# Kernel optimization log

Measured on AMD Instinct MI355X. Metric: run time of the kernel, lower is better.

## Reference

```python
import jax, jax.numpy as jnp
import numpy as np

B, S, H, NH = 2, 2048, 1024, 16
HD = H // NH


def setup_inputs() -> dict:
    key = jax.random.key(0)
    ks = jax.random.split(key, 12)
    query = jax.random.normal(ks[0], (B, S, H), dtype=jnp.float32)
    key_t = jax.random.normal(ks[1], (B, S, H), dtype=jnp.float32)
    value = jax.random.normal(ks[2], (B, S, H), dtype=jnp.float32)
    kpm = jax.random.randint(ks[3], (B, S), 0, 2).astype(bool)
    kpm = kpm.at[:, 0].set(False)  # guarantee at least one unmasked key per row
    bias = jax.random.normal(ks[4], (1, NH, S, S), dtype=jnp.float32)
    init = 0.02
    q_w = jax.random.normal(ks[5], (H, H), dtype=jnp.float32) * init
    k_w = jax.random.normal(ks[6], (H, H), dtype=jnp.float32) * init
    v_w = jax.random.normal(ks[7], (H, H), dtype=jnp.float32) * init
    o_w = jax.random.normal(ks[8], (H, H), dtype=jnp.float32) * init
    q_b = jnp.zeros((H,), jnp.float32)
    k_b = jnp.zeros((H,), jnp.float32)
    v_b = jnp.zeros((H,), jnp.float32)
    o_b = jnp.zeros((H,), jnp.float32)
    return {"query": query, "key": key_t, "value": value,
            "key_padding_mask": kpm, "bias": bias,
            "q_w": q_w, "q_b": q_b, "k_w": k_w, "k_b": k_b,
            "v_w": v_w, "v_b": v_b, "o_w": o_w, "o_b": o_b}


def _shape(x):
    # [B, S, H] -> [B, NH, S, HD]
    b, s, _ = x.shape
    return x.reshape(b, s, NH, HD).transpose(0, 2, 1, 3)


def reference(query, key, value, key_padding_mask, bias,
              q_w, q_b, k_w, k_b, v_w, v_b, o_w, o_b):
    scale = HD ** -0.5
    q = _shape(query @ q_w.T + q_b)
    k = _shape(key @ k_w.T + k_b)
    v = _shape(value @ v_w.T + v_b)
    attn = jnp.einsum('bhqd,bhkd->bhqk', q, k) * scale + bias
    mask = key_padding_mask[:, None, None, :]  # [B,1,1,S]
    attn = jnp.where(mask, -jnp.inf, attn)
    probs = jax.nn.softmax(attn, axis=-1)
    # safe-softmax: zero masked entries and renormalize with clamped denom
    probs = jnp.where(mask, 0.0, probs)
    denom = jnp.maximum(probs.sum(axis=-1, keepdims=True), 1e-6)
    probs = probs / denom
    ctx = jnp.einsum('bhqk,bhkd->bhqd', probs, v)
    ctx = ctx.transpose(0, 2, 1, 3).reshape(query.shape[0], query.shape[1], H)
    return ctx @ o_w.T + o_b
```

## Files before the change

kernel.cpp:

```cpp
#include <hip/hip_runtime.h>
#include <math.h>

#define Ss  2048
#define Hh  1024

typedef unsigned short u16;
typedef __attribute__((ext_vector_type(8))) short short8;
typedef __attribute__((ext_vector_type(4))) float fx4;

__device__ __forceinline__ u16 f2bf(float f) {
  unsigned int u = __float_as_uint(f);
  u = (u + 0x7fffu + ((u >> 16) & 1u)) >> 16;
  return (u16)u;
}

__device__ __forceinline__ void gld_lds16(const u16* g, u16* l) {
  __builtin_amdgcn_global_load_lds(
      (const __attribute__((address_space(1))) unsigned int*)(const unsigned int*)g,
      (__attribute__((address_space(3))) unsigned int*)(unsigned int*)l, 16, 0, 0);
}

#define MFMA16(a,b,c) __builtin_amdgcn_mfma_f32_16x16x32_bf16((a),(b),(c),0,0,0)

__global__ __launch_bounds__(256) void cast3(const float* __restrict__ a,
    const float* __restrict__ b, const float* __restrict__ c,
    u16* __restrict__ oa, u16* __restrict__ ob, u16* __restrict__ oc) {
  const int z = blockIdx.z;
  const float* in = z == 0 ? a : (z == 1 ? b : c);
  u16* out = z == 0 ? oa : (z == 1 ? ob : oc);
  const int i = (blockIdx.x * 256 + threadIdx.x) * 4;
  const float4 v = *(const float4*)(in + i);
  ushort4 r; r.x = f2bf(v.x); r.y = f2bf(v.y); r.z = f2bf(v.z); r.w = f2bf(v.w);
  *(ushort4*)(out + i) = r;
}

__global__ __launch_bounds__(256) void cast4(const float* __restrict__ a,
    const float* __restrict__ b, const float* __restrict__ c, const float* __restrict__ d,
    u16* __restrict__ oa, u16* __restrict__ ob, u16* __restrict__ oc, u16* __restrict__ od) {
  const int z = blockIdx.z;
  const float* in = z == 0 ? a : (z == 1 ? b : (z == 2 ? c : d));
  u16* out = z == 0 ? oa : (z == 1 ? ob : (z == 2 ? oc : od));
  const int i = (blockIdx.x * 256 + threadIdx.x) * 4;
  const float4 v = *(const float4*)(in + i);
  ushort4 r; r.x = f2bf(v.x); r.y = f2bf(v.y); r.z = f2bf(v.z); r.w = f2bf(v.w);
  *(ushort4*)(out + i) = r;
}

__global__ __launch_bounds__(256) void build_maskadd(const int* __restrict__ kpm,
                                                     float* __restrict__ ma) {
  const int i = blockIdx.x * 256 + threadIdx.x;
  ma[i] = kpm[i] ? -1.0e30f : 0.0f;
}

template <int MODE>
__device__ __forceinline__ void gemm_core(const u16* __restrict__ A,
    const u16* __restrict__ W, const float* __restrict__ bias,
    void* __restrict__ out, float scale) {
  __shared__ __align__(16) u16 As[2][4096];
  __shared__ __align__(16) u16 Bs[2][4096];
  const int tid = threadIdx.x;
  const int w = tid >> 6, lane = tid & 63, ln = lane & 15, quad = lane >> 4;
  const int i0 = blockIdx.y * 128, j0 = blockIdx.x * 128;
  const int wr = (w & 1) * 64, wc = (w >> 1) * 64;
  fx4 acc[4][4] = {};
  const int L0 = w * 64 + lane, L1 = L0 + 256;
  const u16* sa0 = A + (size_t)(i0 + (L0 & 127)) * 1024 + (L0 >> 7) * 8;
  const u16* sa1 = A + (size_t)(i0 + (L1 & 127)) * 1024 + (L1 >> 7) * 8;
  const u16* sb0 = W + (size_t)(j0 + (L0 & 127)) * 1024 + (L0 >> 7) * 8;
  const u16* sb1 = W + (size_t)(j0 + (L1 & 127)) * 1024 + (L1 >> 7) * 8;
  const int d0 = (w * 64) * 8, d1 = (256 + w * 64) * 8;

  gld_lds16(sa0, &As[0][d0]); gld_lds16(sa1, &As[0][d1]);
  gld_lds16(sb0, &Bs[0][d0]); gld_lds16(sb1, &Bs[0][d1]);
  __syncthreads();

  for (int k0 = 0; k0 < 1024; k0 += 32) {
    const int cur = (k0 >> 5) & 1;
    if (k0 + 32 < 1024) {
      const int nb = cur ^ 1;
      gld_lds16(sa0 + k0 + 32, &As[nb][d0]); gld_lds16(sa1 + k0 + 32, &As[nb][d1]);
      gld_lds16(sb0 + k0 + 32, &Bs[nb][d0]); gld_lds16(sb1 + k0 + 32, &Bs[nb][d1]);
    }
    short8 a[4], b[4];
#pragma unroll
    for (int t = 0; t < 4; ++t) {
      a[t] = *(const short8*)&As[cur][(quad * 128 + wr + t * 16 + ln) * 8];
      b[t] = *(const short8*)&Bs[cur][(quad * 128 + wc + t * 16 + ln) * 8];
    }
#pragma unroll
    for (int mt = 0; mt < 4; ++mt)
#pragma unroll
      for (int nt = 0; nt < 4; ++nt)
        acc[mt][nt] = MFMA16(a[mt], b[nt], acc[mt][nt]);
    __syncthreads();
  }
#pragma unroll
  for (int nt = 0; nt < 4; ++nt) {
    const int col = j0 + wc + nt * 16 + ln;
    const float bv = bias[col];
#pragma unroll
    for (int mt = 0; mt < 4; ++mt)
#pragma unroll
      for (int r = 0; r < 4; ++r) {
        const int row = i0 + wr + mt * 16 + quad * 4 + r;
        const float val = (acc[mt][nt][r] + bv) * scale;
        if (MODE == 1) {
          const int bb = row >> 11, s = row & 2047, h = col >> 6, d = col & 63;
          ((u16*)out)[((size_t)(bb * 16 + h) * 2048 + s) * 64 + d] = f2bf(val);
        } else {
          ((float*)out)[(size_t)row * 1024 + col] = val;
        }
      }
  }
}

__global__ __launch_bounds__(256) void gemm_qkv(
    const u16* xq, const u16* xk, const u16* xv,
    const u16* wq, const u16* wk, const u16* wv,
    const float* bq, const float* bk, const float* bv,
    u16* q, u16* k, u16* v) {
  const int z = blockIdx.z;
  const u16* A = z == 0 ? xq : (z == 1 ? xk : xv);
  const u16* W = z == 0 ? wq : (z == 1 ? wk : wv);
  const float* bb = z == 0 ? bq : (z == 1 ? bk : bv);
  u16* o = z == 0 ? q : (z == 1 ? k : v);
  const float sc = z == 0 ? 0.125f : 1.0f;
  gemm_core<1>(A, W, bb, o, sc);
}

__global__ __launch_bounds__(256) void gemm_o(const u16* ctx, const u16* wo,
                                              const float* ob, float* out) {
  gemm_core<0>(ctx, wo, ob, out, 1.0f);
}

__global__ __launch_bounds__(256) void transpose_v(const u16* __restrict__ v,
                                                   u16* __restrict__ vt) {
  __shared__ u16 T[64][72];
  const int tid = threadIdx.x;
  const int bh = blockIdx.y, s0 = blockIdx.x * 64;
#pragma unroll
  for (int i = 0; i < 2; ++i) {
    const int L = i * 256 + tid, key = L >> 3, dc = L & 7;
    const uint4 val = *(const uint4*)&v[((size_t)bh * 2048 + s0 + key) * 64 + dc * 8];
    *(uint4*)&T[key][dc * 8] = val;
  }
  __syncthreads();
#pragma unroll
  for (int i = 0; i < 2; ++i) {
    const int L = i * 256 + tid, d = L >> 3, kc = L & 7;
    u16 tmp[8];
#pragma unroll
    for (int j = 0; j < 8; ++j) tmp[j] = T[kc * 8 + j][d];
    *(uint4*)&vt[((size_t)bh * 64 + d) * 2048 + s0 + kc * 8] = *(const uint4*)tmp;
  }
}

__global__ __launch_bounds__(256) void attn(const u16* __restrict__ Qb,
    const u16* __restrict__ Kb, const u16* __restrict__ VT,
    const float* __restrict__ bias, const float* __restrict__ maskadd,
    u16* __restrict__ ctx) {
  __shared__ __align__(16) u16 Ks[2][4096];
  __shared__ __align__(16) u16 Vs[2][4096];
  __shared__ __align__(16) u16 Ps[4096];
  const int tid = threadIdx.x;
  const int w = tid >> 6, lane = tid & 63, ln = lane & 15, quad = lane >> 4;
  const int q0 = blockIdx.x * 64;
  const int hb = blockIdx.y, h = hb >> 1, b = hb & 1, bh = b * 16 + h;
  const int wr = w * 16;

  short8 qf[2];
#pragma unroll
  for (int ks = 0; ks < 2; ++ks)
    qf[ks] = *(const short8*)&Qb[((size_t)bh * 2048 + q0 + wr + ln) * 64 +
                                 ks * 32 + quad * 8];
  float mi = -3.0e38f, li = 0.f;
  fx4 O[4] = {};

  const int L0 = w * 64 + lane, L1 = L0 + 256;
  const u16* sk0 = Kb + ((size_t)bh * 2048 + (L0 & 63)) * 64 + (L0 >> 6) * 8;
  const u16* sk1 = Kb + ((size_t)bh * 2048 + (L1 & 63)) * 64 + (L1 >> 6) * 8;
  const u16* sv0 = VT + ((size_t)bh * 64 + (L0 & 63)) * 2048 + (L0 >> 6) * 8;
  const u16* sv1 = VT + ((size_t)bh * 64 + (L1 & 63)) * 2048 + (L1 >> 6) * 8;
  const int d0 = (w * 64) * 8, d1 = (256 + w * 64) * 8;

  const float* bp = bias + (size_t)h * Ss * Ss + (size_t)(q0 + wr + ln) * Ss + quad * 4;
  const float* mp = maskadd + b * Ss + quad * 4;

  gld_lds16(sk0, &Ks[0][d0]); gld_lds16(sk1, &Ks[0][d1]);
  gld_lds16(sv0, &Vs[0][d0]); gld_lds16(sv1, &Vs[0][d1]);
  fx4 bm[4];
#pragma unroll
  for (int nt = 0; nt < 4; ++nt) {
    const float4 bv = *(const float4*)(bp + nt * 16);
    const float4 mv = *(const float4*)(mp + nt * 16);
    bm[nt][0] = bv.x + mv.x; bm[nt][1] = bv.y + mv.y;
    bm[nt][2] = bv.z + mv.z; bm[nt][3] = bv.w + mv.w;
  }
  __syncthreads();

  for (int kt = 0; kt < Ss; kt += 64) {
    const int cur = (kt >> 6) & 1;
    if (kt + 64 < Ss) {
      const int nb = cur ^ 1;
      gld_lds16(sk0 + (size_t)(kt + 64) * 64, &Ks[nb][d0]);
      gld_lds16(sk1 + (size_t)(kt + 64) * 64, &Ks[nb][d1]);
      gld_lds16(sv0 + kt + 64, &Vs[nb][d0]);
      gld_lds16(sv1 + kt + 64, &Vs[nb][d1]);
    }
    const int kn = (kt + 64 < Ss) ? kt + 64 : kt;
    fx4 bmn[4];
#pragma unroll
    for (int nt = 0; nt < 4; ++nt) {
      const float4 bv = *(const float4*)(bp + kn + nt * 16);
      const float4 mv = *(const float4*)(mp + kn + nt * 16);
      bmn[nt][0] = bv.x + mv.x; bmn[nt][1] = bv.y + mv.y;
      bmn[nt][2] = bv.z + mv.z; bmn[nt][3] = bv.w + mv.w;
    }

    fx4 S[4] = {};
#pragma unroll
    for (int ks = 0; ks < 2; ++ks)
#pragma unroll
      for (int nt = 0; nt < 4; ++nt) {
        const short8 kf = *(const short8*)&Ks[cur][((ks * 4 + quad) * 64 + nt * 16 + ln) * 8];
        S[nt] = MFMA16(kf, qf[ks], S[nt]);
      }

    float pmax = -3.0e38f;
#pragma unroll
    for (int nt = 0; nt < 4; ++nt)
#pragma unroll
      for (int r = 0; r < 4; ++r) {
        S[nt][r] += bm[nt][r];
        pmax = fmaxf(pmax, S[nt][r]);
      }
    pmax = fmaxf(pmax, __shfl_xor(pmax, 16));
    pmax = fmaxf(pmax, __shfl_xor(pmax, 32));

    if (!__all(pmax <= mi + 8.0f)) {
      const float mn = fmaxf(mi, pmax);
      const float a = __expf(mi - mn);
#pragma unroll
      for (int r = 0; r < 4; ++r) {
        const float ar = __shfl(a, quad * 4 + r);
#pragma unroll
        for (int nt = 0; nt < 4; ++nt) O[nt][r] *= ar;
      }
      li *= a;
      mi = mn;
    }

    float rs = 0.f;
#pragma unroll
    for (int nt = 0; nt < 4; ++nt)
#pragma unroll
      for (int r = 0; r < 4; ++r) {
        S[nt][r] = __expf(S[nt][r] - mi);
        rs += S[nt][r];
      }
    rs += __shfl_xor(rs, 16);
    rs += __shfl_xor(rs, 32);
    li += rs;

#pragma unroll
    for (int nt = 0; nt < 4; ++nt) {
      unsigned int u0, u1;
      asm("v_cvt_pk_bf16_f32 %0, %1, %2" : "=v"(u0) : "v"(S[nt][0]), "v"(S[nt][1]));
      asm("v_cvt_pk_bf16_f32 %0, %1, %2" : "=v"(u1) : "v"(S[nt][2]), "v"(S[nt][3]));
      const int kcb = nt * 2 + (quad >> 1);
      uint2 pk; pk.x = u0; pk.y = u1;
      *(uint2*)&Ps[(kcb * 64 + wr + ln) * 8 + (quad & 1) * 4] = pk;
    }

#pragma unroll
    for (int ks = 0; ks < 2; ++ks) {
      const short8 pf = *(const short8*)&Ps[((ks * 4 + quad) * 64 + wr + ln) * 8];
#pragma unroll
      for (int nt = 0; nt < 4; ++nt) {
        const short8 vf = *(const short8*)&Vs[cur][((ks * 4 + quad) * 64 + nt * 16 + ln) * 8];
        O[nt] = MFMA16(pf, vf, O[nt]);
      }
    }

#pragma unroll
    for (int nt = 0; nt < 4; ++nt) bm[nt] = bmn[nt];
    __syncthreads();
  }

#pragma unroll
  for (int r = 0; r < 4; ++r) {
    const float lr = __shfl(li, quad * 4 + r);
    const float inv = 1.0f / fmaxf(lr, 1e-6f);
    const int qg = q0 + wr + quad * 4 + r;
#pragma unroll
    for (int nt = 0; nt < 4; ++nt)
      ctx[((size_t)(b * Ss + qg)) * 1024 + h * 64 + nt * 16 + ln] =
          f2bf(O[nt][r] * inv);
  }
}

extern "C" void kernel_launch(void* const* d_in, const int* in_sizes, int n_in,
                              void* d_out, int out_size, void* d_ws, size_t ws_size,
                              hipStream_t stream) {
  const float* query = (const float*)d_in[0];
  const float* key   = (const float*)d_in[1];
  const float* value = (const float*)d_in[2];
  const int*   kpm   = (const int*)d_in[3];
  const float* bias  = (const float*)d_in[4];
  const float* q_w   = (const float*)d_in[5];
  const float* q_b   = (const float*)d_in[6];
  const float* k_w   = (const float*)d_in[7];
  const float* k_b   = (const float*)d_in[8];
  const float* v_w   = (const float*)d_in[9];
  const float* v_b   = (const float*)d_in[10];
  const float* o_w   = (const float*)d_in[11];
  const float* o_b   = (const float*)d_in[12];
  float* out = (float*)d_out;

  char* ws = (char*)d_ws;
  const size_t MB = 1024 * 1024;
  u16* xq = (u16*)(ws + 0 * MB);
  u16* xk = (u16*)(ws + 8 * MB);
  u16* xv = (u16*)(ws + 16 * MB);
  u16* wq = (u16*)(ws + 24 * MB);
  u16* wk = (u16*)(ws + 26 * MB);
  u16* wv = (u16*)(ws + 28 * MB);
  u16* wo = (u16*)(ws + 30 * MB);
  u16* qb = (u16*)(ws + 32 * MB);
  u16* kb = (u16*)(ws + 40 * MB);
  u16* vb = (u16*)(ws + 48 * MB);
  u16* cx = (u16*)(ws + 56 * MB);
  u16* vt = (u16*)(ws + 0 * MB);
  float* ma = (float*)(ws + 8 * MB);

  cast3<<<dim3(4096, 1, 3), 256, 0, stream>>>(query, key, value, xq, xk, xv);
  cast4<<<dim3(1024, 1, 4), 256, 0, stream>>>(q_w, k_w, v_w, o_w, wq, wk, wv, wo);
  gemm_qkv<<<dim3(8, 32, 3), 256, 0, stream>>>(xq, xk, xv, wq, wk, wv,
                                               q_b, k_b, v_b, qb, kb, vb);
  transpose_v<<<dim3(32, 32), 256, 0, stream>>>(vb, vt);
  build_maskadd<<<dim3(16), 256, 0, stream>>>(kpm, ma);
  attn<<<dim3(32, 32), 256, 0, stream>>>(qb, kb, vt, bias, ma, cx);
  gemm_o<<<dim3(8, 32), 256, 0, stream>>>(cx, wo, o_b, out);
}
```

Measured before the change: 598.1 us.

## Load K fragments directly from global in attention, fuse cast and mask kernels

The attention kernel stops staging K tiles through LDS and instead loads each lane's K MFMA fragments straight from global memory into registers. This frees LDS (the Ks buffer) and adds a launch_bounds occupancy hint of 4 blocks. The separate cast kernels are merged into one prep launch, and the mask-add kernel is removed by converting the key padding mask inline inside attention. These changes aim to cut launch overhead and LDS traffic, at the cost of uncoalesced, unpipelined global K loads that the loop may stall on.

```diff
diff --git a/kernel.cpp b/kernel.cpp
--- a/kernel.cpp
+++ b/kernel.cpp
@@ -22,34 +22,29 @@
 
 #define MFMA16(a,b,c) __builtin_amdgcn_mfma_f32_16x16x32_bf16((a),(b),(c),0,0,0)
 
-__global__ __launch_bounds__(256) void cast3(const float* __restrict__ a,
-    const float* __restrict__ b, const float* __restrict__ c,
-    u16* __restrict__ oa, u16* __restrict__ ob, u16* __restrict__ oc) {
-  const int z = blockIdx.z;
-  const float* in = z == 0 ? a : (z == 1 ? b : c);
-  u16* out = z == 0 ? oa : (z == 1 ? ob : oc);
-  const int i = (blockIdx.x * 256 + threadIdx.x) * 4;
-  const float4 v = *(const float4*)(in + i);
-  ushort4 r; r.x = f2bf(v.x); r.y = f2bf(v.y); r.z = f2bf(v.z); r.w = f2bf(v.w);
+__global__ __launch_bounds__(256) void prep(
+    const float* __restrict__ q, const float* __restrict__ k,
+    const float* __restrict__ v, const float* __restrict__ wq,
+    const float* __restrict__ wk, const float* __restrict__ wv,
+    const float* __restrict__ wo,
+    u16* __restrict__ oq, u16* __restrict__ ok, u16* __restrict__ ov,
+    u16* __restrict__ owq, u16* __restrict__ owk, u16* __restrict__ owv,
+    u16* __restrict__ owo) {
+  const int bid = blockIdx.x;
+  const float* in; u16* out; int x;
+  if (bid < 12288) {
+    const int z = bid >> 12; x = bid & 4095;
+    in = z == 0 ? q : (z == 1 ? k : v);
+    out = z == 0 ? oq : (z == 1 ? ok : ov);
+  } else {
+    const int t = bid - 12288, z = t >> 10; x = t & 1023;
+    in = z == 0 ? wq : (z == 1 ? wk : (z == 2 ? wv : wo));
+    out = z == 0 ? owq : (z == 1 ? owk : (z == 2 ? owv : owo));
+  }
+  const int i = (x * 256 + threadIdx.x) * 4;
+  const float4 vv = *(const float4*)(in + i);
+  ushort4 r; r.x = f2bf(vv.x); r.y = f2bf(vv.y); r.z = f2bf(vv.z); r.w = f2bf(vv.w);
   *(ushort4*)(out + i) = r;
-}
-
-__global__ __launch_bounds__(256) void cast4(const float* __restrict__ a,
-    const float* __restrict__ b, const float* __restrict__ c, const float* __restrict__ d,
-    u16* __restrict__ oa, u16* __restrict__ ob, u16* __restrict__ oc, u16* __restrict__ od) {
-  const int z = blockIdx.z;
-  const float* in = z == 0 ? a : (z == 1 ? b : (z == 2 ? c : d));
-  u16* out = z == 0 ? oa : (z == 1 ? ob : (z == 2 ? oc : od));
-  const int i = (blockIdx.x * 256 + threadIdx.x) * 4;
-  const float4 v = *(const float4*)(in + i);
-  ushort4 r; r.x = f2bf(v.x); r.y = f2bf(v.y); r.z = f2bf(v.z); r.w = f2bf(v.w);
-  *(ushort4*)(out + i) = r;
-}
-
-__global__ __launch_bounds__(256) void build_maskadd(const int* __restrict__ kpm,
-                                                     float* __restrict__ ma) {
-  const int i = blockIdx.x * 256 + threadIdx.x;
-  ma[i] = kpm[i] ? -1.0e30f : 0.0f;
 }
 
 template <int MODE>
@@ -155,11 +150,10 @@
   }
 }
 
-__global__ __launch_bounds__(256) void attn(const u16* __restrict__ Qb,
+__global__ __launch_bounds__(256, 4) void attn(const u16* __restrict__ Qb,
     const u16* __restrict__ Kb, const u16* __restrict__ VT,
-    const float* __restrict__ bias, const float* __restrict__ maskadd,
+    const float* __restrict__ bias, const int* __restrict__ kpm,
     u16* __restrict__ ctx) {
-  __shared__ __align__(16) u16 Ks[2][4096];
   __shared__ __align__(16) u16 Vs[2][4096];
   __shared__ __align__(16) u16 Ps[4096];
   const int tid = threadIdx.x;
@@ -177,24 +171,24 @@
   fx4 O[4] = {};
 
   const int L0 = w * 64 + lane, L1 = L0 + 256;
-  const u16* sk0 = Kb + ((size_t)bh * 2048 + (L0 & 63)) * 64 + (L0 >> 6) * 8;
-  const u16* sk1 = Kb + ((size_t)bh * 2048 + (L1 & 63)) * 64 + (L1 >> 6) * 8;
   const u16* sv0 = VT + ((size_t)bh * 64 + (L0 & 63)) * 2048 + (L0 >> 6) * 8;
   const u16* sv1 = VT + ((size_t)bh * 64 + (L1 & 63)) * 2048 + (L1 >> 6) * 8;
   const int d0 = (w * 64) * 8, d1 = (256 + w * 64) * 8;
 
+  const u16* kb_l = Kb + ((size_t)bh * 2048 + ln) * 64 + quad * 8;
   const float* bp = bias + (size_t)h * Ss * Ss + (size_t)(q0 + wr + ln) * Ss + quad * 4;
-  const float* mp = maskadd + b * Ss + quad * 4;
-
-  gld_lds16(sk0, &Ks[0][d0]); gld_lds16(sk1, &Ks[0][d1]);
+  const int* mp = kpm + b * Ss + quad * 4;
+
   gld_lds16(sv0, &Vs[0][d0]); gld_lds16(sv1, &Vs[0][d1]);
   fx4 bm[4];
 #pragma unroll
   for (int nt = 0; nt < 4; ++nt) {
     const float4 bv = *(const float4*)(bp + nt * 16);
-    const float4 mv = *(const float4*)(mp + nt * 16);
-    bm[nt][0] = bv.x + mv.x; bm[nt][1] = bv.y + mv.y;
-    bm[nt][2] = bv.z + mv.z; bm[nt][3] = bv.w + mv.w;
+    const int4 mv = *(const int4*)(mp + nt * 16);
+    bm[nt][0] = bv.x + (mv.x ? -1.0e30f : 0.0f);
+    bm[nt][1] = bv.y + (mv.y ? -1.0e30f : 0.0f);
+    bm[nt][2] = bv.z + (mv.z ? -1.0e30f : 0.0f);
+    bm[nt][3] = bv.w + (mv.w ? -1.0e30f : 0.0f);
   }
   __syncthreads();
 
@@ -202,8 +196,6 @@
     const int cur = (kt >> 6) & 1;
     if (kt + 64 < Ss) {
       const int nb = cur ^ 1;
-      gld_lds16(sk0 + (size_t)(kt + 64) * 64, &Ks[nb][d0]);
-      gld_lds16(sk1 + (size_t)(kt + 64) * 64, &Ks[nb][d1]);
       gld_lds16(sv0 + kt + 64, &Vs[nb][d0]);
       gld_lds16(sv1 + kt + 64, &Vs[nb][d1]);
     }
@@ -212,19 +204,27 @@
 #pragma unroll
     for (int nt = 0; nt < 4; ++nt) {
       const float4 bv = *(const float4*)(bp + kn + nt * 16);
-      const float4 mv = *(const float4*)(mp + kn + nt * 16);
-      bmn[nt][0] = bv.x + mv.x; bmn[nt][1] = bv.y + mv.y;
-      bmn[nt][2] = bv.z + mv.z; bmn[nt][3] = bv.w + mv.w;
-    }
+      const int4 mv = *(const int4*)(mp + kn + nt * 16);
+      bmn[nt][0] = bv.x + (mv.x ? -1.0e30f : 0.0f);
+      bmn[nt][1] = bv.y + (mv.y ? -1.0e30f : 0.0f);
+      bmn[nt][2] = bv.z + (mv.z ? -1.0e30f : 0.0f);
+      bmn[nt][3] = bv.w + (mv.w ? -1.0e30f : 0.0f);
+    }
+
+    short8 kf[2][4];
+    const u16* kp8 = kb_l + (size_t)kt * 64;
+#pragma unroll
+    for (int ks = 0; ks < 2; ++ks)
+#pragma unroll
+      for (int nt = 0; nt < 4; ++nt)
+        kf[ks][nt] = *(const short8*)(kp8 + nt * 1024 + ks * 32);
 
     fx4 S[4] = {};
 #pragma unroll
     for (int ks = 0; ks < 2; ++ks)
 #pragma unroll
-      for (int nt = 0; nt < 4; ++nt) {
-        const short8 kf = *(const short8*)&Ks[cur][((ks * 4 + quad) * 64 + nt * 16 + ln) * 8];
-        S[nt] = MFMA16(kf, qf[ks], S[nt]);
-      }
+      for (int nt = 0; nt < 4; ++nt)
+        S[nt] = MFMA16(kf[ks][nt], qf[ks], S[nt]);
 
     float pmax = -3.0e38f;
 #pragma unroll
@@ -331,14 +331,12 @@
   u16* vb = (u16*)(ws + 48 * MB);
   u16* cx = (u16*)(ws + 56 * MB);
   u16* vt = (u16*)(ws + 0 * MB);
-  float* ma = (float*)(ws + 8 * MB);
-
-  cast3<<<dim3(4096, 1, 3), 256, 0, stream>>>(query, key, value, xq, xk, xv);
-  cast4<<<dim3(1024, 1, 4), 256, 0, stream>>>(q_w, k_w, v_w, o_w, wq, wk, wv, wo);
+
+  prep<<<dim3(16384), 256, 0, stream>>>(query, key, value, q_w, k_w, v_w, o_w,
+                                        xq, xk, xv, wq, wk, wv, wo);
   gemm_qkv<<<dim3(8, 32, 3), 256, 0, stream>>>(xq, xk, xv, wq, wk, wv,
                                                q_b, k_b, v_b, qb, kb, vb);
   transpose_v<<<dim3(32, 32), 256, 0, stream>>>(vb, vt);
-  build_maskadd<<<dim3(16), 256, 0, stream>>>(kpm, ma);
-  attn<<<dim3(32, 32), 256, 0, stream>>>(qb, kb, vt, bias, ma, cx);
+  attn<<<dim3(32, 32), 256, 0, stream>>>(qb, kb, vt, bias, kpm, cx);
   gemm_o<<<dim3(8, 32), 256, 0, stream>>>(cx, wo, o_b, out);
 }
```

Result: slower. 666.8 us (+11.5%).
